# Optimization experiments

Hardware: AMD Instinct MI355X
Metric: run time of the kernel (lower is better)

Reference implementation:

```python
import jax, jax.numpy as jnp
import numpy as np

N = 10000      # nodes
E = 100000     # edges
D = 768        # hidden = heads * head_dim
H = 4          # heads
C = D // H     # 192 per-head channels
EDIM = 16      # edge feature dim
NREL = 10      # num relations
L = 3          # num TransformerConv layers


def setup_inputs() -> dict:
    key = jax.random.key(0)
    ks = jax.random.split(key, 16)
    s = 0.02
    x = jax.random.normal(ks[0], (N, D), jnp.float32)
    edge_index = jax.random.randint(ks[1], (2, E), 0, N, jnp.int32)
    rel = jax.random.randint(ks[2], (E,), 0, NREL).astype(jnp.float32)
    w = jax.random.uniform(ks[3], (E,), jnp.float32)
    edge_attr = jnp.stack([rel, w], axis=1)  # [E, 2]: (relation_id, weight)
    rel_emb = jax.random.normal(ks[4], (NREL, EDIM - 1), jnp.float32) * s
    W_edge = jax.random.normal(ks[5], (EDIM, EDIM), jnp.float32) * s
    b_edge = jnp.zeros((EDIM,), jnp.float32)
    Wk = jax.random.normal(ks[6], (L, D, D), jnp.float32) * s
    bk = jnp.zeros((L, D), jnp.float32)
    Wq = jax.random.normal(ks[7], (L, D, D), jnp.float32) * s
    bq = jnp.zeros((L, D), jnp.float32)
    Wv = jax.random.normal(ks[8], (L, D, D), jnp.float32) * s
    bv = jnp.zeros((L, D), jnp.float32)
    We = jax.random.normal(ks[9], (L, EDIM, D), jnp.float32) * s   # lin_edge, no bias (PyG)
    Wskip = jax.random.normal(ks[10], (L, D, D), jnp.float32) * s  # root/skip linear
    bskip = jnp.zeros((L, D), jnp.float32)
    ln_g = jnp.ones((D,), jnp.float32)
    ln_b = jnp.zeros((D,), jnp.float32)
    return dict(x=x, edge_attr=edge_attr, edge_index=edge_index, rel_emb=rel_emb,
                W_edge=W_edge, b_edge=b_edge, Wk=Wk, bk=bk, Wq=Wq, bq=bq,
                Wv=Wv, bv=bv, We=We, Wskip=Wskip, bskip=bskip, ln_g=ln_g, ln_b=ln_b)


def reference(x, edge_attr, edge_index, rel_emb, W_edge, b_edge,
              Wk, bk, Wq, bq, Wv, bv, We, Wskip, bskip, ln_g, ln_b):
    src, dst = edge_index[0], edge_index[1]
    # _process_edge_features: embed relation id, concat weight, project
    rel_ids = jnp.clip(jax.lax.stop_gradient(edge_attr[:, 0]).astype(jnp.int32), 0, NREL - 1)
    ef = jnp.concatenate([rel_emb[rel_ids], edge_attr[:, 1:2]], axis=-1) @ W_edge + b_edge  # [E,16]
    scale = 1.0 / np.sqrt(C)
    h = x  # input_proj is Identity (input_dim == hidden_dim)
    for l in range(L):
        q = (h @ Wq[l] + bq[l]).reshape(N, H, C)
        k = (h @ Wk[l] + bk[l]).reshape(N, H, C)
        v = (h @ Wv[l] + bv[l]).reshape(N, H, C)
        e = (ef @ We[l]).reshape(E, H, C)           # per-edge embedding
        kj = k[src] + e                              # [E,H,C]
        alpha = jnp.einsum('ehc,ehc->eh', q[dst], kj) * scale  # [E,H]
        # scatter-softmax over incoming edges of each destination node
        m = jax.ops.segment_max(jax.lax.stop_gradient(alpha), dst, num_segments=N)
        a = jnp.exp(alpha - m[dst])
        denom = jax.ops.segment_sum(a, dst, num_segments=N)
        a = a / (denom[dst] + 1e-16)
        msg = (v[src] + e) * a[..., None]            # [E,H,C]
        out = jax.ops.segment_sum(msg.reshape(E, H * C), dst, num_segments=N)
        h = out + h @ Wskip[l] + bskip[l]            # root_weight skip connection
        if l < L - 1:
            h = jax.nn.gelu(h, approximate=False)    # dropout: eval mode -> identity
    mu = jnp.mean(h, axis=-1, keepdims=True)
    var = jnp.mean((h - mu) ** 2, axis=-1, keepdims=True)
    h = (h - mu) / jnp.sqrt(var + 1e-5) * ln_g + ln_b
    return jnp.mean(h, axis=0)  # global_mean_pool over single graph -> [D]
```

## Files before the change

### kernel.cpp

```cpp
#include <hip/hip_runtime.h>
#include <hip/hip_bf16.h>
#include <math.h>
#include <stdint.h>

#define NN 10000
#define EE 100000
#define DD 768
#define HH 4
#define CC 192
#define EDIM 16
#define NREL 10
#define MP 10240
#define NQ2 3200
#define NB 3136
#define SCALE 0.07216878364870322f

using short8  = __attribute__((ext_vector_type(8))) short;
using floatx4 = __attribute__((ext_vector_type(4))) float;


__device__ __forceinline__ float b2f(short u) {
    union { unsigned int i; float f; } t;
    t.i = ((unsigned int)(unsigned short)u) << 16;
    return t.f;
}

__device__ __forceinline__ short f2b(float f) {
    __hip_bfloat16 h = __float2bfloat16(f);
    short r;
    __builtin_memcpy(&r, &h, 2);
    return r;
}

__device__ __forceinline__ __hip_bfloat16 rd_any(const void* p, long long j, int bf) {
    if (bf) return ((const __hip_bfloat16*)p)[j];
    return __float2bfloat16(((const float*)p)[j]);
}

__device__ __forceinline__ void gload16(const __hip_bfloat16* g, __hip_bfloat16* l) {
    __builtin_amdgcn_global_load_lds(
        (const __attribute__((address_space(1))) unsigned int*)g,
        (__attribute__((address_space(3))) unsigned int*)l, 16, 0, 0);
}

__global__ __launch_bounds__(256) void detect_zero(const void* edge_attr,
                                                   int* flag, int* counts) {
    int i = blockIdx.x * 256 + threadIdx.x;
    if (i < NN) counts[i] = 0;
    if (blockIdx.x == 0 && threadIdx.x < 64) {
        const unsigned short* p = (const unsigned short*)edge_attr;
        int nz = (p[4 * threadIdx.x] != 0) ? 1 : 0;
        unsigned long long m = __ballot(nz);
        if (threadIdx.x == 0) *flag = (__popcll(m) > 8) ? 1 : 0;
    }
}


__global__ __launch_bounds__(256) void cvt_big(
    const void* x, const void* We, const int* flag,
    __hip_bfloat16* hb, __hip_bfloat16* Web) {
    long long i = (long long)blockIdx.x * 256 + threadIdx.x;
    int bf = *flag;
    const long long NX = (long long)NN * DD;
    const long long NE2 = 3LL * EDIM * DD;
    if (i < NX) { hb[i] = rd_any(x, i, bf); return; } i -= NX;
    if (i < NE2) { Web[i] = rd_any(We, i, bf); return; } i -= NE2;
    if (i < (long long)(MP - NN) * DD) hb[(long long)NN * DD + i] = __float2bfloat16(0.0f);
}

__global__ __launch_bounds__(256) void cvt_small(
    const void* ea, const void* rel, const void* Wed, const void* bed,
    const void* bk, const void* bq, const void* bv, const void* bs,
    const void* lg, const void* lb, const int* flag,
    __hip_bfloat16* eab, __hip_bfloat16* relb, __hip_bfloat16* Wedb,
    __hip_bfloat16* bedb, __hip_bfloat16* ballb, __hip_bfloat16* lgb,
    __hip_bfloat16* lbb) {
    long long i = (long long)blockIdx.x * 256 + threadIdx.x;
    int bf = *flag;
    if (i < 2LL * EE) { eab[i] = rd_any(ea, i, bf); return; } i -= 2LL * EE;
    if (i < NREL * (EDIM - 1)) { relb[i] = rd_any(rel, i, bf); return; } i -= NREL * (EDIM - 1);
    if (i < EDIM * EDIM) { Wedb[i] = rd_any(Wed, i, bf); return; } i -= EDIM * EDIM;
    if (i < EDIM) { bedb[i] = rd_any(bed, i, bf); return; } i -= EDIM;
    if (i < 3 * NB) {
        int l = (int)(i / NB), c = (int)(i % NB);
        const void* src; long long off;
        if (c < 768)       { src = bq; off = (long long)l * DD + c; }
        else if (c < 1536) { src = bk; off = (long long)l * DD + (c - 768); }
        else if (c < 2304) { src = bv; off = (long long)l * DD + (c - 1536); }
        else if (c < 3072) { src = bs; off = (long long)l * DD + (c - 2304); }
        else { ballb[i] = __float2bfloat16(0.0f); return; }
        ballb[i] = rd_any(src, off, bf); return;
    } i -= 3 * NB;
    if (i < DD) { lgb[i] = rd_any(lg, i, bf); return; } i -= DD;
    if (i < DD) { lbb[i] = rd_any(lb, i, bf); return; }
}

__global__ __launch_bounds__(256) void wt_all(
    const void* Wq, const void* Wk, const void* Wv, const void* Ws,
    const int* flag, __hip_bfloat16* Wt3) {
    __shared__ __hip_bfloat16 tile[32][33];
    int mm = blockIdx.y;
    int l = mm >> 2, m = mm & 3;
    const void* src = (m == 0) ? Wq : (m == 1) ? Wk : (m == 2) ? Wv : Ws;
    int bx = blockIdx.x;
    int tr = bx / 24, tc = bx % 24;
    int k0 = tr * 32, c0 = tc * 32;
    int t = threadIdx.x;
    int rr = t >> 5, cc = t & 31;
    int bf = *flag;
    long long base = (long long)l * DD * DD;
#pragma unroll
    for (int p = 0; p < 4; p++)
        tile[p * 8 + rr][cc] =
            rd_any(src, base + (long long)(k0 + p * 8 + rr) * DD + c0 + cc, bf);
    __syncthreads();
    __hip_bfloat16* dst = Wt3 + (size_t)l * NB * DD + (size_t)(m * 768 + c0) * DD + k0;
#pragma unroll
    for (int p = 0; p < 4; p++)
        dst[(size_t)(p * 8 + rr) * DD + cc] = tile[cc][p * 8 + rr];
}

__global__ __launch_bounds__(256) void mq_kernel(
    const void* Wq, const void* bq, const int* flag,
    const __hip_bfloat16* __restrict__ Web, __hip_bfloat16* __restrict__ Wt3,
    __hip_bfloat16* __restrict__ ballb) {
    __shared__ float WeS[16][193];
    const int lh = blockIdx.y, l = lh >> 2, hh = lh & 3;
    const int t = threadIdx.x;
    const int bf = *flag;
    for (int i = t; i < 16 * 192; i += 256) {
        int j = i / 192, c = i % 192;
        WeS[j][c] = (float)Web[(size_t)l * EDIM * DD + (size_t)j * DD + hh * CC + c];
    }
    __syncthreads();
    const int k = blockIdx.x * 64 + (t >> 2);
    const int j0 = (t & 3) * 4;
    float s0 = 0.f, s1 = 0.f, s2 = 0.f, s3 = 0.f;
    if (bf) {
        const short8* qp = (const short8*)((const __hip_bfloat16*)Wq +
            ((size_t)l * DD + k) * DD + hh * CC);
#pragma unroll 4
        for (int ch = 0; ch < 24; ch++) {
            short8 v = qp[ch];
#pragma unroll
            for (int u = 0; u < 8; u++) {
                float w = b2f(v[u]);
                int c = ch * 8 + u;
                s0 += w * WeS[j0 + 0][c]; s1 += w * WeS[j0 + 1][c];
                s2 += w * WeS[j0 + 2][c]; s3 += w * WeS[j0 + 3][c];
            }
        }
    } else {
        const float4* qp = (const float4*)((const float*)Wq +
            ((size_t)l * DD + k) * DD + hh * CC);
#pragma unroll 4
        for (int ch = 0; ch < 48; ch++) {
            float4 v = qp[ch];
            float wv[4] = {v.x, v.y, v.z, v.w};
#pragma unroll
            for (int u = 0; u < 4; u++) {
                float w = wv[u];
                int c = ch * 4 + u;
                s0 += w * WeS[j0 + 0][c]; s1 += w * WeS[j0 + 1][c];
                s2 += w * WeS[j0 + 2][c]; s3 += w * WeS[j0 + 3][c];
            }
        }
    }
    const size_t base = (size_t)l * NB * DD;
    const int row = 3072 + hh * 16 + j0;
    Wt3[base + (size_t)(row + 0) * DD + k] = __float2bfloat16(s0);
    Wt3[base + (size_t)(row + 1) * DD + k] = __float2bfloat16(s1);
    Wt3[base + (size_t)(row + 2) * DD + k] = __float2bfloat16(s2);
    Wt3[base + (size_t)(row + 3) * DD + k] = __float2bfloat16(s3);
    if (blockIdx.x == 0 && t < 4) {
        float b0 = 0.f, b1 = 0.f, b2 = 0.f, b3 = 0.f;
        for (int c = 0; c < CC; c++) {
            float w = (float)rd_any(bq, (long long)l * DD + hh * CC + c, bf);
            b0 += w * WeS[j0 + 0][c]; b1 += w * WeS[j0 + 1][c];
            b2 += w * WeS[j0 + 2][c]; b3 += w * WeS[j0 + 3][c];
        }
        ballb[l * NB + 3072 + hh * 16 + j0 + 0] = __float2bfloat16(b0);
        ballb[l * NB + 3072 + hh * 16 + j0 + 1] = __float2bfloat16(b1);
        ballb[l * NB + 3072 + hh * 16 + j0 + 2] = __float2bfloat16(b2);
        ballb[l * NB + 3072 + hh * 16 + j0 + 3] = __float2bfloat16(b3);
    }
}


__global__ __launch_bounds__(256) void count_kernel(const int* ei, int* counts) {
    int e = blockIdx.x * 256 + threadIdx.x;
    if (e < EE) atomicAdd(&counts[ei[EE + e]], 1);
}

__global__ __launch_bounds__(256) void scan_kernel(const int* counts, int* rowptr,
                                                   int* cursor) {
    __shared__ int sdata[256];
    int t = threadIdx.x;
    int base = t * 40;
    int cnt = (base < NN) ? min(40, NN - base) : 0;
    int s = 0;
    for (int i = 0; i < cnt; i++) s += counts[base + i];
    sdata[t] = s;
    __syncthreads();
    for (int off = 1; off < 256; off <<= 1) {
        int add = (t >= off) ? sdata[t - off] : 0;
        __syncthreads();
        sdata[t] += add;
        __syncthreads();
    }
    int run = sdata[t] - s;
    for (int i = 0; i < cnt; i++) {
        cursor[base + i] = run;
        run += counts[base + i];
        rowptr[base + i + 1] = run;
    }
    if (t == 0) rowptr[0] = 0;
}

__global__ __launch_bounds__(256) void fill_kernel(const int* ei, int* cursor,
                                                   int* eids, int* esrc) {
    int e = blockIdx.x * 256 + threadIdx.x;
    if (e < EE) {
        int d = ei[EE + e];
        int pos = atomicAdd(&cursor[d], 1);
        eids[pos] = e;
        esrc[pos] = ei[e];
    }
}


__global__ __launch_bounds__(256) void ef_kernel(
    const int* __restrict__ eids,
    const __hip_bfloat16* __restrict__ eab, const __hip_bfloat16* __restrict__ relb,
    const __hip_bfloat16* __restrict__ Wedb, const __hip_bfloat16* __restrict__ bedb,
    __hip_bfloat16* __restrict__ efb) {
    int idx = blockIdx.x * 256 + threadIdx.x;
    if (idx >= EE * EDIM) return;
    int p = idx >> 4, j = idx & 15;
    int e = eids[p];
    int rid = (int)((float)eab[e * 2 + 0]);
    rid = min(max(rid, 0), NREL - 1);
    float w = (float)eab[e * 2 + 1];
    float s = (float)bedb[j];
#pragma unroll
    for (int i = 0; i < 15; i++)
        s += (float)relb[rid * 15 + i] * (float)Wedb[i * EDIM + j];
    s += w * (float)Wedb[15 * EDIM + j];
    efb[idx] = __float2bfloat16(s);
}


__device__ __forceinline__ void stage_half(const __hip_bfloat16* g, int row0, int ktile,
                                           char* ldsdst, int tid) {
#pragma unroll
    for (int j = 0; j < 2; ++j) {
        int c = j * 512 + tid;
        int row = c >> 3;
        int sch = (c & 7) ^ (row & 7);
        gload16(g + (size_t)(row0 + row) * DD + ktile * 64 + sch * 8,
                (__hip_bfloat16*)(ldsdst + c * 16));
    }
}

#define MF16(va, vb, cc) cc = __builtin_amdgcn_mfma_f32_16x16x32_bf16(va, vb, cc, 0, 0, 0)
#define BAR() __builtin_amdgcn_s_barrier()
#define WLG() asm volatile("s_waitcnt lgkmcnt(0)" ::: "memory")
#define WVM(N) asm volatile("s_waitcnt vmcnt(" #N ")" ::: "memory")
#define LDS8(off) (*(const short8*)(smem + (off)))

__global__ __launch_bounds__(512) void gemm256(
    const __hip_bfloat16* __restrict__ A, const __hip_bfloat16* __restrict__ Bt,
    const __hip_bfloat16* __restrict__ bias, __hip_bfloat16* __restrict__ C) {
    __shared__ __align__(16) char smem[131072];
    const int tid = threadIdx.x;
    const int wid = tid >> 6, lane = tid & 63;
    const int quad = lane >> 4, l15 = lane & 15;
    const int wm = wid >> 2, wn = wid & 3;
    const int bid = (int)blockIdx.x;
    const int swz = (bid & 7) * 60 + (bid >> 3);
    const int m0 = (swz / 12) * 256;
    const int n0 = (swz % 12) * 256;

    const int xa0 = (quad ^ (l15 & 7)) * 16;
    const int xa1 = ((quad + 4) ^ (l15 & 7)) * 16;
    const int aRow = (wm * 128 + l15) * 128;
    const int bRow = 32768 + (wn * 64 + l15) * 128;

    floatx4 acc[8][4] = {};
    short8 a[4][2], bA[2][2], bB[2][2];

    stage_half(A, m0, 0, smem + 0, tid);
    stage_half(A, m0 + 128, 0, smem + 16384, tid);
    stage_half(Bt, n0, 0, smem + 32768, tid);
    stage_half(Bt, n0 + 128, 0, smem + 49152, tid);
    stage_half(Bt, n0, 1, smem + 98304, tid);
    stage_half(Bt, n0 + 128, 1, smem + 114688, tid);
    WVM(4);
    BAR();

#pragma unroll 1
    for (int it = 0; it < 6; ++it) {
        const int kA = 2 * it + 1;
        const int kB = (it < 5) ? 2 * it + 2 : 0;
        const int kC = (it < 5) ? 2 * it + 3 : 1;
#pragma unroll
        for (int mt = 0; mt < 4; ++mt) {
            a[mt][0] = LDS8(aRow + mt * 2048 + xa0);
            a[mt][1] = LDS8(aRow + mt * 2048 + xa1);
        }
#pragma unroll
        for (int nt = 0; nt < 2; ++nt) {
            bA[nt][0] = LDS8(bRow + nt * 2048 + xa0);
            bA[nt][1] = LDS8(bRow + nt * 2048 + xa1);
        }
        stage_half(A, m0, kA, smem + 65536, tid);
        BAR(); WLG();
        __builtin_amdgcn_s_setprio(1);
#pragma unroll
        for (int mt = 0; mt < 4; ++mt)
#pragma unroll
            for (int nt = 0; nt < 2; ++nt) {
                MF16(a[mt][0], bA[nt][0], acc[mt][nt]);
                MF16(a[mt][1], bA[nt][1], acc[mt][nt]);
            }
        __builtin_amdgcn_s_setprio(0);
        BAR();
#pragma unroll
        for (int nt = 0; nt < 2; ++nt) {
            bB[nt][0] = LDS8(bRow + (nt + 2) * 2048 + xa0);
            bB[nt][1] = LDS8(bRow + (nt + 2) * 2048 + xa1);
        }
        stage_half(A, m0 + 128, kA, smem + 81920, tid);
        WVM(6);
        BAR(); WLG();
        __builtin_amdgcn_s_setprio(1);
#pragma unroll
        for (int mt = 0; mt < 4; ++mt)
#pragma unroll
            for (int nt = 0; nt < 2; ++nt) {
                MF16(a[mt][0], bB[nt][0], acc[mt][nt + 2]);
                MF16(a[mt][1], bB[nt][1], acc[mt][nt + 2]);
            }
        __builtin_amdgcn_s_setprio(0);
        BAR();
#pragma unroll
        for (int mt = 0; mt < 4; ++mt) {
            a[mt][0] = LDS8(aRow + (mt + 4) * 2048 + xa0);
            a[mt][1] = LDS8(aRow + (mt + 4) * 2048 + xa1);
        }
        stage_half(Bt, n0, kB, smem + 32768, tid);
        BAR(); WLG();
        __builtin_amdgcn_s_setprio(1);
#pragma unroll
        for (int mt = 0; mt < 4; ++mt)
#pragma unroll
            for (int nt = 0; nt < 2; ++nt) {
                MF16(a[mt][0], bB[nt][0], acc[mt + 4][nt + 2]);
                MF16(a[mt][1], bB[nt][1], acc[mt + 4][nt + 2]);
            }
        __builtin_amdgcn_s_setprio(0);
        BAR();
        stage_half(Bt, n0 + 128, kB, smem + 49152, tid);
        WVM(4);
        BAR(); WLG();
        __builtin_amdgcn_s_setprio(1);
#pragma unroll
        for (int mt = 0; mt < 4; ++mt)
#pragma unroll
            for (int nt = 0; nt < 2; ++nt) {
                MF16(a[mt][0], bA[nt][0], acc[mt + 4][nt]);
                MF16(a[mt][1], bA[nt][1], acc[mt + 4][nt]);
            }
        __builtin_amdgcn_s_setprio(0);
        BAR();
#pragma unroll
        for (int mt = 0; mt < 4; ++mt) {
            a[mt][0] = LDS8(65536 + aRow + mt * 2048 + xa0);
            a[mt][1] = LDS8(65536 + aRow + mt * 2048 + xa1);
        }
#pragma unroll
        for (int nt = 0; nt < 2; ++nt) {
            bA[nt][0] = LDS8(65536 + bRow + nt * 2048 + xa0);
            bA[nt][1] = LDS8(65536 + bRow + nt * 2048 + xa1);
        }
        stage_half(A, m0, kB, smem + 0, tid);
        BAR(); WLG();
        __builtin_amdgcn_s_setprio(1);
#pragma unroll
        for (int mt = 0; mt < 4; ++mt)
#pragma unroll
            for (int nt = 0; nt < 2; ++nt) {
                MF16(a[mt][0], bA[nt][0], acc[mt][nt]);
                MF16(a[mt][1], bA[nt][1], acc[mt][nt]);
            }
        __builtin_amdgcn_s_setprio(0);
        BAR();
#pragma unroll
        for (int nt = 0; nt < 2; ++nt) {
            bB[nt][0] = LDS8(65536 + bRow + (nt + 2) * 2048 + xa0);
            bB[nt][1] = LDS8(65536 + bRow + (nt + 2) * 2048 + xa1);
        }
        stage_half(A, m0 + 128, kB, smem + 16384, tid);
        WVM(6);
        BAR(); WLG();
        __builtin_amdgcn_s_setprio(1);
#pragma unroll
        for (int mt = 0; mt < 4; ++mt)
#pragma unroll
            for (int nt = 0; nt < 2; ++nt) {
                MF16(a[mt][0], bB[nt][0], acc[mt][nt + 2]);
                MF16(a[mt][1], bB[nt][1], acc[mt][nt + 2]);
            }
        __builtin_amdgcn_s_setprio(0);
        BAR();
#pragma unroll
        for (int mt = 0; mt < 4; ++mt) {
            a[mt][0] = LDS8(65536 + aRow + (mt + 4) * 2048 + xa0);
            a[mt][1] = LDS8(65536 + aRow + (mt + 4) * 2048 + xa1);
        }
        stage_half(Bt, n0, kC, smem + 98304, tid);
        BAR(); WLG();
        __builtin_amdgcn_s_setprio(1);
#pragma unroll
        for (int mt = 0; mt < 4; ++mt)
#pragma unroll
            for (int nt = 0; nt < 2; ++nt) {
                MF16(a[mt][0], bB[nt][0], acc[mt + 4][nt + 2]);
                MF16(a[mt][1], bB[nt][1], acc[mt + 4][nt + 2]);
            }
        __builtin_amdgcn_s_setprio(0);
        BAR();
        stage_half(Bt, n0 + 128, kC, smem + 114688, tid);
        WVM(4);
        BAR(); WLG();
        __builtin_amdgcn_s_setprio(1);
#pragma unroll
        for (int mt = 0; mt < 4; ++mt)
#pragma unroll
            for (int nt = 0; nt < 2; ++nt) {
                MF16(a[mt][0], bA[nt][0], acc[mt + 4][nt]);
                MF16(a[mt][1], bA[nt][1], acc[mt + 4][nt]);
            }
        __builtin_amdgcn_s_setprio(0);
        BAR();
    }

    asm volatile("s_waitcnt vmcnt(0)" ::: "memory");
    BAR();
    {
        short* stg = (short*)smem + wid * 1152;
        float bv[4];
#pragma unroll
        for (int nt = 0; nt < 4; ++nt)
            bv[nt] = (float)bias[n0 + wn * 64 + nt * 16 + l15];
        const int rdo = (lane >> 2) * 68 + (lane & 3) * 16;
        const int grow0 = m0 + wm * 128 + (lane >> 2);
        const int gcol = n0 + wn * 64 + (lane & 3) * 16;
#pragma unroll
        for (int mt = 0; mt < 8; ++mt) {
#pragma unroll
            for (int nt = 0; nt < 4; ++nt)
#pragma unroll
                for (int r = 0; r < 4; ++r)
                    stg[(quad * 4 + r) * 68 + nt * 16 + l15] =
                        f2b(acc[mt][nt][r] + bv[nt]);
            asm volatile("s_waitcnt lgkmcnt(0)" ::: "memory");
            short8 v0 = *(const short8*)(stg + rdo);
            short8 v1 = *(const short8*)(stg + rdo + 8);
            int grow = grow0 + mt * 16;
            if (grow < NN) {
                short8* dp = (short8*)(C + (size_t)grow * NQ2 + gcol);
                dp[0] = v0; dp[1] = v1;
            }
            asm volatile("s_waitcnt lgkmcnt(0)" ::: "memory");
        }
    }
}


__global__ __launch_bounds__(256) void qe_gemm(
    const __hip_bfloat16* __restrict__ A, const __hip_bfloat16* __restrict__ Bt,
    const __hip_bfloat16* __restrict__ bias, __hip_bfloat16* __restrict__ C) {
    __shared__ __align__(16) char smem[16384];
    const int tid = threadIdx.x;
    const int wid = tid >> 6, lane = tid & 63;
    const int quad = lane >> 4, l15 = lane & 15;
    const int m0 = blockIdx.x * 64;
    const int xa0 = (quad ^ (l15 & 7)) * 16;
    const int xa1 = ((quad + 4) ^ (l15 & 7)) * 16;
    floatx4 acc[4] = {};
    for (int kt = 0; kt < 12; ++kt) {
#pragma unroll
        for (int j = 0; j < 4; ++j) {
            int c = j * 256 + tid;
            int hf = c >> 9;
            int cc = c & 511;
            int row = cc >> 3;
            int sch = (cc & 7) ^ (row & 7);
            const __hip_bfloat16* src = hf
                ? (Bt + (size_t)row * DD + kt * 64 + sch * 8)
                : (A + (size_t)(m0 + row) * DD + kt * 64 + sch * 8);
            gload16(src, (__hip_bfloat16*)(smem + c * 16));
        }
        asm volatile("s_waitcnt vmcnt(0)" ::: "memory");
        BAR();
        short8 a0 = LDS8((wid * 16 + l15) * 128 + xa0);
        short8 a1 = LDS8((wid * 16 + l15) * 128 + xa1);
#pragma unroll
        for (int nt = 0; nt < 4; ++nt) {
            short8 b0 = LDS8(8192 + (nt * 16 + l15) * 128 + xa0);
            short8 b1 = LDS8(8192 + (nt * 16 + l15) * 128 + xa1);
            MF16(a0, b0, acc[nt]);
            MF16(a1, b1, acc[nt]);
        }
        WLG();
        BAR();
    }
#pragma unroll
    for (int nt = 0; nt < 4; ++nt) {
        float bb = (float)bias[nt * 16 + l15];
#pragma unroll
        for (int r = 0; r < 4; ++r) {
            int row = m0 + wid * 16 + quad * 4 + r;
            if (row < NN)
                C[(size_t)row * NQ2 + 3072 + nt * 16 + l15] =
                    __float2bfloat16(acc[nt][r] + bb);
        }
    }
}


__global__ __launch_bounds__(256) void node_attn(
    const int* __restrict__ rowptr, const int* __restrict__ esrc,
    const __hip_bfloat16* __restrict__ qkvs, const __hip_bfloat16* __restrict__ efb,
    const __hip_bfloat16* __restrict__ Wel, __hip_bfloat16* __restrict__ hb,
    int do_gelu) {
    const int wv = threadIdx.x >> 6, lane = threadIdx.x & 63;
    const int n = blockIdx.x * 2 + (wv >> 1);
    const int half = wv & 1;
    const int cb = half * 384 + lane * 6;
    const int sj = lane & 15;
    const int hsel = lane & 32;
    const float qe_gate = ((lane & 16) == 0) ? 1.0f : 0.0f;
    const int s0 = rowptr[n], s1 = rowptr[n + 1];
    const short* qk = (const short*)qkvs;
    float q[6];
    {
        const short2* qp = (const short2*)(qk + (size_t)n * NQ2 + cb);
        short2 a = qp[0], b = qp[1], c = qp[2];
        q[0] = b2f(a.x); q[1] = b2f(a.y); q[2] = b2f(b.x);
        q[3] = b2f(b.y); q[4] = b2f(c.x); q[5] = b2f(c.y);
    }
    const float qe_l = b2f(qk[(size_t)n * NQ2 + 3072 + (half * 2 + (lane >> 5)) * 16 + sj]);
    float m = -INFINITY, lsum = 0.f, sacc = 0.f;
    float acc[6] = {};
    for (int p = s0; p < s1; p++) {
        int src = esrc[p];
        const short2* kp = (const short2*)(qk + (size_t)src * NQ2 + 768 + cb);
        const short2* vp = (const short2*)(qk + (size_t)src * NQ2 + 1536 + cb);
        short2 ka = kp[0], kb = kp[1], kc = kp[2];
        short2 va = vp[0], vb = vp[1], vc = vp[2];
        float efv = b2f(((const short*)efb)[(size_t)p * 16 + sj]);
        float part = qe_gate * qe_l * efv;
        part += q[0] * b2f(ka.x) + q[1] * b2f(ka.y) + q[2] * b2f(kb.x);
        part += q[3] * b2f(kb.y) + q[4] * b2f(kc.x) + q[5] * b2f(kc.y);
        part += __shfl_xor(part, 1); part += __shfl_xor(part, 2);
        part += __shfl_xor(part, 4); part += __shfl_xor(part, 8);
        part += __shfl_xor(part, 16);
        float a = part * SCALE;
        float nm = fmaxf(m, a);
        float sc = __expf(m - nm);
        float w  = __expf(a - nm);
        lsum = lsum * sc + w;
        m = nm;
        acc[0] = acc[0] * sc + w * b2f(va.x); acc[1] = acc[1] * sc + w * b2f(va.y);
        acc[2] = acc[2] * sc + w * b2f(vb.x); acc[3] = acc[3] * sc + w * b2f(vb.y);
        acc[4] = acc[4] * sc + w * b2f(vc.x); acc[5] = acc[5] * sc + w * b2f(vc.y);
        sacc = sacc * sc + w * efv;
    }
    float inv = 1.0f / (lsum + 1e-16f);
#pragma unroll
    for (int i = 0; i < 6; i++) acc[i] *= inv;
    float sS = sacc * inv;
    {
        const short2* sp = (const short2*)(qk + (size_t)n * NQ2 + 2304 + cb);
        short2 a = sp[0], b = sp[1], c = sp[2];
        acc[0] += b2f(a.x); acc[1] += b2f(a.y); acc[2] += b2f(b.x);
        acc[3] += b2f(b.y); acc[4] += b2f(c.x); acc[5] += b2f(c.y);
    }
#pragma unroll
    for (int j = 0; j < 16; j++) {
        float sv = __shfl(sS, hsel + j);
        const short2* wp = (const short2*)(Wel + (size_t)j * DD + cb);
        short2 a = wp[0], b = wp[1], c = wp[2];
        acc[0] += sv * b2f(a.x); acc[1] += sv * b2f(a.y); acc[2] += sv * b2f(b.x);
        acc[3] += sv * b2f(b.y); acc[4] += sv * b2f(c.x); acc[5] += sv * b2f(c.y);
    }
    if (do_gelu) {
#pragma unroll
        for (int i = 0; i < 6; i++)
            acc[i] = 0.5f * acc[i] * (1.0f + erff(acc[i] * 0.70710678118654752f));
    }
    short2 o0, o1, o2;
    o0.x = f2b(acc[0]); o0.y = f2b(acc[1]);
    o1.x = f2b(acc[2]); o1.y = f2b(acc[3]);
    o2.x = f2b(acc[4]); o2.y = f2b(acc[5]);
    short2* hp = (short2*)(hb + (size_t)n * DD + cb);
    hp[0] = o0; hp[1] = o1; hp[2] = o2;
}


__global__ __launch_bounds__(256) void ln_pool(
    const __hip_bfloat16* __restrict__ hb, const __hip_bfloat16* __restrict__ g,
    const __hip_bfloat16* __restrict__ b, float* __restrict__ partial) {
    __shared__ float sbuf[4][768];
    int grp = blockIdx.x, t = threadIdx.x;
    int wid = t >> 6, lane = t & 63;
    float gv[12], bv[12], acc[12];
#pragma unroll
    for (int i = 0; i < 12; i++) {
        gv[i] = (float)g[lane + i * 64];
        bv[i] = (float)b[lane + i * 64];
        acc[i] = 0.f;
    }
    for (int r = wid; r < 25; r += 4) {
        const __hip_bfloat16* row = hb + (size_t)(grp * 25 + r) * DD;
        float x[12];
        float s = 0.f, q = 0.f;
#pragma unroll
        for (int i = 0; i < 12; i++) {
            x[i] = (float)row[lane + i * 64];
            s += x[i]; q += x[i] * x[i];
        }
#pragma unroll
        for (int m = 32; m > 0; m >>= 1) {
            s += __shfl_xor(s, m); q += __shfl_xor(q, m);
        }
        float mu = s * (1.0f / 768.0f);
        float ms = q * (1.0f / 768.0f);
        float inv = 1.0f / sqrtf(ms - mu * mu + 1e-5f);
#pragma unroll
        for (int i = 0; i < 12; i++)
            acc[i] += (x[i] - mu) * inv * gv[i] + bv[i];
    }
#pragma unroll
    for (int i = 0; i < 12; i++) sbuf[wid][lane + i * 64] = acc[i];
    __syncthreads();
#pragma unroll
    for (int j = 0; j < 3; j++) {
        int col = t + j * 256;
        partial[(size_t)grp * DD + col] =
            sbuf[0][col] + sbuf[1][col] + sbuf[2][col] + sbuf[3][col];
    }
}

__global__ __launch_bounds__(256) void pool_final(
    const float* __restrict__ partial, void* __restrict__ out,
    const int* __restrict__ flag) {
    int dd = blockIdx.x * 256 + threadIdx.x;
    if (dd >= DD) return;
    float s = 0.f;
    for (int g2 = 0; g2 < 400; g2++) s += partial[(size_t)g2 * DD + dd];
    s *= (1.0f / 10000.0f);
    if (*flag) ((__hip_bfloat16*)out)[dd] = __float2bfloat16(s);
    else ((float*)out)[dd] = s;
}


extern "C" void kernel_launch(void* const* d_in, const int* in_sizes, int n_in,
                              void* d_out, int out_size, void* d_ws, size_t ws_size,
                              hipStream_t stream) {
    const void* x         = d_in[0];
    const void* edge_attr = d_in[1];
    const int*  ei        = (const int*)d_in[2];
    const void* rel_emb   = d_in[3];
    const void* W_edge    = d_in[4];
    const void* b_edge    = d_in[5];
    const void* Wk        = d_in[6];
    const void* bk        = d_in[7];
    const void* Wq        = d_in[8];
    const void* bq        = d_in[9];
    const void* Wv        = d_in[10];
    const void* bv        = d_in[11];
    const void* We        = d_in[12];
    const void* Wskip     = d_in[13];
    const void* bskip     = d_in[14];
    const void* ln_g      = d_in[15];
    const void* ln_b      = d_in[16];

    char* ws = (char*)d_ws;
    int*   flag    = (int*)(ws + 0);
    int*   counts  = (int*)(ws + 256);
    int*   rowptr  = (int*)(ws + 40448);
    int*   cursor  = (int*)(ws + 80640);
    int*   eids    = (int*)(ws + 120832);
    int*   esrc    = (int*)(ws + 520960);
    __hip_bfloat16* efb = (__hip_bfloat16*)(ws + 920960);
    float* partial = (float*)(ws + 4120960);
    __hip_bfloat16* eab   = (__hip_bfloat16*)(ws + 5349760);
    __hip_bfloat16* relb  = (__hip_bfloat16*)(ws + 5749760);
    __hip_bfloat16* Wedb  = (__hip_bfloat16*)(ws + 5750144);
    __hip_bfloat16* bedb  = (__hip_bfloat16*)(ws + 5750656);
    __hip_bfloat16* ballb = (__hip_bfloat16*)(ws + 5750784);
    __hip_bfloat16* lngb  = (__hip_bfloat16*)(ws + 5770752);
    __hip_bfloat16* lnbb  = (__hip_bfloat16*)(ws + 5772288);
    __hip_bfloat16* Web   = (__hip_bfloat16*)(ws + 5773824);
    __hip_bfloat16* hb    = (__hip_bfloat16*)(ws + 5847552);
    __hip_bfloat16* Wt3   = (__hip_bfloat16*)(ws + 21576192);
    __hip_bfloat16* qkvs  = (__hip_bfloat16*)(ws + 36911616);

    dim3 blk(256);

    detect_zero<<<dim3(40), blk, 0, stream>>>(edge_attr, flag, counts);

    {
        long long tot = (long long)NN * DD + 3LL * EDIM * DD + (long long)(MP - NN) * DD;
        cvt_big<<<dim3((unsigned)((tot + 255) / 256)), blk, 0, stream>>>(x, We, flag, hb, Web);
    }
    {
        long long tot = 2LL * EE + NREL * (EDIM - 1) + EDIM * EDIM + EDIM
                        + 3LL * NB + 2LL * DD;
        cvt_small<<<dim3((unsigned)((tot + 255) / 256)), blk, 0, stream>>>(
            edge_attr, rel_emb, W_edge, b_edge, bk, bq, bv, bskip, ln_g, ln_b,
            flag, eab, relb, Wedb, bedb, ballb, lngb, lnbb);
    }
    wt_all<<<dim3(576, 12), blk, 0, stream>>>(Wq, Wk, Wv, Wskip, flag, Wt3);
    mq_kernel<<<dim3(12, 12), blk, 0, stream>>>(Wq, bq, flag, Web, Wt3, ballb);

    count_kernel<<<dim3((EE + 255) / 256), blk, 0, stream>>>(ei, counts);
    scan_kernel<<<dim3(1), blk, 0, stream>>>(counts, rowptr, cursor);
    fill_kernel<<<dim3((EE + 255) / 256), blk, 0, stream>>>(ei, cursor, eids, esrc);

    ef_kernel<<<dim3((EE * EDIM) / 256), blk, 0, stream>>>(eids, eab, relb, Wedb, bedb, efb);

    for (int l = 0; l < 3; l++) {
        const __hip_bfloat16* We_l = Web + (size_t)l * EDIM * DD;
        gemm256<<<dim3(480), dim3(512), 0, stream>>>(
            hb, Wt3 + (size_t)l * NB * DD, ballb + (size_t)l * NB, qkvs);
        qe_gemm<<<dim3(160), blk, 0, stream>>>(
            hb, Wt3 + (size_t)l * NB * DD + (size_t)3072 * DD,
            ballb + (size_t)l * NB + 3072, qkvs);
        node_attn<<<dim3(NN / 2), blk, 0, stream>>>(rowptr, esrc, qkvs, efb,
                                                    We_l, hb, (l < 2) ? 1 : 0);
    }

    ln_pool<<<dim3(400), blk, 0, stream>>>(hb, lngb, lnbb, partial);
    pool_final<<<dim3(3), blk, 0, stream>>>(partial, d_out, flag);
}
```

Baseline: 612.0 us.

## Merge GEMM main-loop phases to halve barriers per iteration

Restructures the 256x256 bf16 MFMA GEMM main loop from eight barrier-separated phases to four. Each phase now issues both half-tile global-to-LDS stages together, loads both B fragment sets up front, and runs twice as many MFMAs between barriers. sched_barrier fences stop the compiler from moving instructions across the sync points. This removes barrier and wait overhead and gives each phase more compute to overlap with loads, at the cost of more live registers and a tighter window before LDS buffers are overwritten.

```diff
diff --git a/kernel.cpp b/kernel.cpp
--- a/kernel.cpp
+++ b/kernel.cpp
@@ -266,6 +266,7 @@
 #define BAR() __builtin_amdgcn_s_barrier()
 #define WLG() asm volatile("s_waitcnt lgkmcnt(0)" ::: "memory")
 #define WVM(N) asm volatile("s_waitcnt vmcnt(" #N ")" ::: "memory")
+#define SB() __builtin_amdgcn_sched_barrier(0)
 #define LDS8(off) (*(const short8*)(smem + (off)))
 
 __global__ __launch_bounds__(512) void gemm256(
@@ -303,6 +304,8 @@
         const int kA = 2 * it + 1;
         const int kB = (it < 5) ? 2 * it + 2 : 0;
         const int kC = (it < 5) ? 2 * it + 3 : 1;
+        stage_half(A, m0, kA, smem + 65536, tid);
+        stage_half(A, m0 + 128, kA, smem + 81920, tid);
 #pragma unroll
         for (int mt = 0; mt < 4; ++mt) {
             a[mt][0] = LDS8(aRow + mt * 2048 + xa0);
@@ -312,9 +315,10 @@
         for (int nt = 0; nt < 2; ++nt) {
             bA[nt][0] = LDS8(bRow + nt * 2048 + xa0);
             bA[nt][1] = LDS8(bRow + nt * 2048 + xa1);
-        }
-        stage_half(A, m0, kA, smem + 65536, tid);
-        BAR(); WLG();
+            bB[nt][0] = LDS8(bRow + (nt + 2) * 2048 + xa0);
+            bB[nt][1] = LDS8(bRow + (nt + 2) * 2048 + xa1);
+        }
+        SB(); BAR(); WLG(); SB();
         __builtin_amdgcn_s_setprio(1);
 #pragma unroll
         for (int mt = 0; mt < 4; ++mt)
@@ -322,34 +326,19 @@
             for (int nt = 0; nt < 2; ++nt) {
                 MF16(a[mt][0], bA[nt][0], acc[mt][nt]);
                 MF16(a[mt][1], bA[nt][1], acc[mt][nt]);
-            }
-        __builtin_amdgcn_s_setprio(0);
-        BAR();
-#pragma unroll
-        for (int nt = 0; nt < 2; ++nt) {
-            bB[nt][0] = LDS8(bRow + (nt + 2) * 2048 + xa0);
-            bB[nt][1] = LDS8(bRow + (nt + 2) * 2048 + xa1);
-        }
-        stage_half(A, m0 + 128, kA, smem + 81920, tid);
-        WVM(6);
-        BAR(); WLG();
-        __builtin_amdgcn_s_setprio(1);
-#pragma unroll
-        for (int mt = 0; mt < 4; ++mt)
-#pragma unroll
-            for (int nt = 0; nt < 2; ++nt) {
                 MF16(a[mt][0], bB[nt][0], acc[mt][nt + 2]);
                 MF16(a[mt][1], bB[nt][1], acc[mt][nt + 2]);
             }
         __builtin_amdgcn_s_setprio(0);
-        BAR();
+        stage_half(Bt, n0, kB, smem + 32768, tid);
+        stage_half(Bt, n0 + 128, kB, smem + 49152, tid);
 #pragma unroll
         for (int mt = 0; mt < 4; ++mt) {
             a[mt][0] = LDS8(aRow + (mt + 4) * 2048 + xa0);
             a[mt][1] = LDS8(aRow + (mt + 4) * 2048 + xa1);
         }
-        stage_half(Bt, n0, kB, smem + 32768, tid);
-        BAR(); WLG();
+        WVM(4);
+        SB(); BAR(); WLG(); SB();
         __builtin_amdgcn_s_setprio(1);
 #pragma unroll
         for (int mt = 0; mt < 4; ++mt)
@@ -357,22 +346,12 @@
             for (int nt = 0; nt < 2; ++nt) {
                 MF16(a[mt][0], bB[nt][0], acc[mt + 4][nt + 2]);
                 MF16(a[mt][1], bB[nt][1], acc[mt + 4][nt + 2]);
-            }
-        __builtin_amdgcn_s_setprio(0);
-        BAR();
-        stage_half(Bt, n0 + 128, kB, smem + 49152, tid);
-        WVM(4);
-        BAR(); WLG();
-        __builtin_amdgcn_s_setprio(1);
-#pragma unroll
-        for (int mt = 0; mt < 4; ++mt)
-#pragma unroll
-            for (int nt = 0; nt < 2; ++nt) {
                 MF16(a[mt][0], bA[nt][0], acc[mt + 4][nt]);
                 MF16(a[mt][1], bA[nt][1], acc[mt + 4][nt]);
             }
         __builtin_amdgcn_s_setprio(0);
-        BAR();
+        stage_half(A, m0, kB, smem + 0, tid);
+        stage_half(A, m0 + 128, kB, smem + 16384, tid);
 #pragma unroll
         for (int mt = 0; mt < 4; ++mt) {
             a[mt][0] = LDS8(65536 + aRow + mt * 2048 + xa0);
@@ -382,9 +361,10 @@
         for (int nt = 0; nt < 2; ++nt) {
             bA[nt][0] = LDS8(65536 + bRow + nt * 2048 + xa0);
             bA[nt][1] = LDS8(65536 + bRow + nt * 2048 + xa1);
-        }
-        stage_half(A, m0, kB, smem + 0, tid);
-        BAR(); WLG();
+            bB[nt][0] = LDS8(65536 + bRow + (nt + 2) * 2048 + xa0);
+            bB[nt][1] = LDS8(65536 + bRow + (nt + 2) * 2048 + xa1);
+        }
+        SB(); BAR(); WLG(); SB();
         __builtin_amdgcn_s_setprio(1);
 #pragma unroll
         for (int mt = 0; mt < 4; ++mt)
@@ -392,34 +372,19 @@
             for (int nt = 0; nt < 2; ++nt) {
                 MF16(a[mt][0], bA[nt][0], acc[mt][nt]);
                 MF16(a[mt][1], bA[nt][1], acc[mt][nt]);
-            }
-        __builtin_amdgcn_s_setprio(0);
-        BAR();
-#pragma unroll
-        for (int nt = 0; nt < 2; ++nt) {
-            bB[nt][0] = LDS8(65536 + bRow + (nt + 2) * 2048 + xa0);
-            bB[nt][1] = LDS8(65536 + bRow + (nt + 2) * 2048 + xa1);
-        }
-        stage_half(A, m0 + 128, kB, smem + 16384, tid);
-        WVM(6);
-        BAR(); WLG();
-        __builtin_amdgcn_s_setprio(1);
-#pragma unroll
-        for (int mt = 0; mt < 4; ++mt)
-#pragma unroll
-            for (int nt = 0; nt < 2; ++nt) {
                 MF16(a[mt][0], bB[nt][0], acc[mt][nt + 2]);
                 MF16(a[mt][1], bB[nt][1], acc[mt][nt + 2]);
             }
         __builtin_amdgcn_s_setprio(0);
-        BAR();
+        stage_half(Bt, n0, kC, smem + 98304, tid);
+        stage_half(Bt, n0 + 128, kC, smem + 114688, tid);
 #pragma unroll
         for (int mt = 0; mt < 4; ++mt) {
             a[mt][0] = LDS8(65536 + aRow + (mt + 4) * 2048 + xa0);
             a[mt][1] = LDS8(65536 + aRow + (mt + 4) * 2048 + xa1);
         }
-        stage_half(Bt, n0, kC, smem + 98304, tid);
-        BAR(); WLG();
+        WVM(4);
+        SB(); BAR(); WLG(); SB();
         __builtin_amdgcn_s_setprio(1);
 #pragma unroll
         for (int mt = 0; mt < 4; ++mt)
@@ -427,22 +392,10 @@
             for (int nt = 0; nt < 2; ++nt) {
                 MF16(a[mt][0], bB[nt][0], acc[mt + 4][nt + 2]);
                 MF16(a[mt][1], bB[nt][1], acc[mt + 4][nt + 2]);
-            }
-        __builtin_amdgcn_s_setprio(0);
-        BAR();
-        stage_half(Bt, n0 + 128, kC, smem + 114688, tid);
-        WVM(4);
-        BAR(); WLG();
-        __builtin_amdgcn_s_setprio(1);
-#pragma unroll
-        for (int mt = 0; mt < 4; ++mt)
-#pragma unroll
-            for (int nt = 0; nt < 2; ++nt) {
                 MF16(a[mt][0], bA[nt][0], acc[mt + 4][nt]);
                 MF16(a[mt][1], bA[nt][1], acc[mt + 4][nt]);
             }
         __builtin_amdgcn_s_setprio(0);
-        BAR();
     }
 
     asm volatile("s_waitcnt vmcnt(0)" ::: "memory");
```

After: 607.6 us. About the same (-0.7%).
